# Kernel tuning notes

Measured on AMD Instinct MI355X. Metric: run time of the kernel, lower is better.

## Reference

```python
import jax, jax.numpy as jnp
import numpy as np

NUM_NODES = 100000
NUM_EDGES = 3200000
D_IN, D_HID, D_OUT = 64, 64, 32


def setup_inputs() -> dict:
    key = jax.random.key(0)
    k1, k2, k3, k4, k5 = jax.random.split(key, 5)
    edge_index = jax.random.randint(k1, (2, NUM_EDGES), 0, NUM_NODES, dtype=jnp.int64)
    edge_weight = jax.random.uniform(k2, (NUM_EDGES,), dtype=jnp.float32)
    emb = jax.random.normal(k3, (NUM_NODES, D_IN), dtype=jnp.float32)
    # glorot-ish scaled weights for the two GCNConv layers
    W1 = jax.random.normal(k4, (D_IN, D_HID), dtype=jnp.float32) * (1.0 / np.sqrt(D_IN))
    b1 = jnp.zeros((D_HID,), dtype=jnp.float32)
    W2 = jax.random.normal(k5, (D_HID, D_OUT), dtype=jnp.float32) * (1.0 / np.sqrt(D_HID))
    b2 = jnp.zeros((D_OUT,), dtype=jnp.float32)
    return {"edge_index": edge_index, "edge_weight": edge_weight,
            "emb": emb, "W1": W1, "b1": b1, "W2": W2, "b2": b2}


def reference(edge_index, edge_weight, emb, W1, b1, W2, b2):
    N = emb.shape[0]
    row, col = edge_index[0], edge_index[1]
    # PyG gcn_norm: add self-loops (weight 1.0), symmetric normalization
    loop = jnp.arange(N, dtype=edge_index.dtype)
    row_f = jnp.concatenate([row, loop])
    col_f = jnp.concatenate([col, loop])
    ew_f = jnp.concatenate([edge_weight, jnp.ones((N,), dtype=edge_weight.dtype)])
    deg = jax.ops.segment_sum(ew_f, col_f, num_segments=N)          # [N]
    deg_inv_sqrt = jnp.where(deg > 0, jax.lax.rsqrt(deg), 0.0)      # inf -> 0
    norm = deg_inv_sqrt[row_f] * ew_f * deg_inv_sqrt[col_f]         # [E+N]

    def gcn_conv(x, W, b):
        x = x @ W                                                    # [N, d_out]
        msg = x[row_f] * norm[:, None]                               # [E+N, d_out]
        out = jax.ops.segment_sum(msg, col_f, num_segments=N)       # [N, d_out]
        return out + b

    x = jax.nn.relu(gcn_conv(emb, W1, b1))
    x = gcn_conv(x, W2, b2)
    # F.normalize(p=2, dim=1, eps=1e-12)
    l2 = jnp.linalg.norm(x, axis=1, keepdims=True)
    return x / jnp.maximum(l2, 1e-12)
```

## Files before the change

### kernel.cpp

```cpp
#include <hip/hip_runtime.h>
#include <hip/hip_fp16.h>
#include <math.h>

#define THREADS 256
#define BWIDTH 512
#define BSHIFT 9
#define CHUNK 3125

__global__ void init_kernel(const int* __restrict__ ei32, int* __restrict__ flag,
                            unsigned int* __restrict__ gcnt) {
    int t = threadIdx.x;
    gcnt[t] = 0u;
    if (t == 0) {
        int z = (ei32[1] == 0) + (ei32[3] == 0) + (ei32[5] == 0) + (ei32[7] == 0);
        *flag = (z == 4) ? 1 : 0;
    }
}

__device__ __forceinline__ int edge_at(const void* ei, int is64, size_t idx) {
    return is64 ? (int)((const long long*)ei)[idx] : ((const int*)ei)[idx];
}

__global__ void p1_count_kernel(const void* __restrict__ ei, const int* __restrict__ flag,
                                unsigned int* __restrict__ gcnt, unsigned int* __restrict__ table,
                                int E, int B) {
    __shared__ unsigned int lcnt[256];
    int t = threadIdx.x, b = blockIdx.x;
    lcnt[t] = 0u;
    __syncthreads();
    int is64 = *flag;
    int base = b * CHUNK;
    int end = min(E, base + CHUNK);
    for (int e = base + t; e < end; e += THREADS) {
        int c = edge_at(ei, is64, (size_t)E + e);
        atomicAdd(&lcnt[c >> BSHIFT], 1u);
    }
    __syncthreads();
    if (t < B) table[(size_t)b * 256 + t] = atomicAdd(&gcnt[t], lcnt[t]);
}

__global__ void p2_scan_kernel(const unsigned int* __restrict__ gcnt,
                               unsigned int* __restrict__ bstart, int B, int E) {
    int t = threadIdx.x;
    unsigned int v = (t < B) ? gcnt[t] : 0u;
    unsigned int incl = v;
    int lane = t & 63, wid = t >> 6;
#pragma unroll
    for (int off = 1; off < 64; off <<= 1) {
        unsigned int x = __shfl_up(incl, off);
        if (lane >= off) incl += x;
    }
    __shared__ unsigned int ws4[4];
    if (lane == 63) ws4[wid] = incl;
    __syncthreads();
    unsigned int wb = 0;
    for (int w = 0; w < wid; ++w) wb += ws4[w];
    unsigned int excl = wb + incl - v;
    if (t < B) bstart[t] = excl;
    if (t == 0) bstart[B] = (unsigned int)E;
}

__global__ void p3_scatter_kernel(const void* __restrict__ ei, const float* __restrict__ ew,
                                  const int* __restrict__ flag,
                                  const unsigned int* __restrict__ bstart,
                                  const unsigned int* __restrict__ table,
                                  int2* __restrict__ out, int E, int B) {
    __shared__ int2 stage[CHUNK];
    __shared__ unsigned char lbin[CHUNK];
    __shared__ unsigned short perm[CHUNK];
    __shared__ unsigned int lcnt[256];
    __shared__ unsigned int lstart[256];
    __shared__ unsigned int lcur[256];
    __shared__ int shiftb[256];
    __shared__ unsigned int ws4[4];

    int t = threadIdx.x, b = blockIdx.x;
    lcnt[t] = 0u;
    __syncthreads();
    int is64 = *flag;
    int base = b * CHUNK;
    int end = min(E, base + CHUNK);
    int n = end - base;
    for (int i = t; i < n; i += THREADS) {
        int e = base + i;
        int r = edge_at(ei, is64, (size_t)e);
        int c = edge_at(ei, is64, (size_t)E + e);
        int bin = c >> BSHIFT;
        stage[i] = make_int2(r | ((c & (BWIDTH - 1)) << 17), __float_as_int(ew[e]));
        lbin[i] = (unsigned char)bin;
        atomicAdd(&lcnt[bin], 1u);
    }
    __syncthreads();
    unsigned int v = lcnt[t];
    unsigned int incl = v;
    int lane = t & 63, wid = t >> 6;
#pragma unroll
    for (int off = 1; off < 64; off <<= 1) {
        unsigned int x = __shfl_up(incl, off);
        if (lane >= off) incl += x;
    }
    if (lane == 63) ws4[wid] = incl;
    __syncthreads();
    unsigned int wb = 0;
    for (int w = 0; w < wid; ++w) wb += ws4[w];
    unsigned int excl = wb + incl - v;
    lstart[t] = excl;
    lcur[t] = excl;
    shiftb[t] = (t < B) ? ((int)(bstart[t] + table[(size_t)b * 256 + t]) - (int)excl) : 0;
    __syncthreads();
    for (int i = t; i < n; i += THREADS) {
        unsigned int pos = atomicAdd(&lcur[lbin[i]], 1u);
        perm[pos] = (unsigned short)i;
    }
    __syncthreads();
    for (int k = t; k < n; k += THREADS) {
        int i = perm[k];
        int bin = lbin[i];
        out[(size_t)(shiftb[bin] + k)] = stage[i];
    }
}

__global__ void p5_bucket_kernel(const int2* __restrict__ bucketed,
                                 const unsigned int* __restrict__ bstart,
                                 float* __restrict__ dinv, int* __restrict__ colptr,
                                 int2* __restrict__ csr, int N, int E) {
    __shared__ unsigned int cnt[BWIDTH];
    __shared__ float deg[BWIDTH];
    __shared__ unsigned int cur[BWIDTH];
    __shared__ unsigned int ws4[4];

    int t = threadIdx.x, b = blockIdx.x;
    cnt[t] = 0u; cnt[t + 256] = 0u;
    deg[t] = 0.f; deg[t + 256] = 0.f;
    __syncthreads();
    unsigned int s = bstart[b], e2 = bstart[b + 1];
    for (unsigned int j = s + t; j < e2; j += THREADS) {
        int2 v = bucketed[j];
        unsigned int cl = ((unsigned int)v.x) >> 17;
        atomicAdd(&cnt[cl], 1u);
        atomicAdd(&deg[cl], __int_as_float(v.y));
    }
    __syncthreads();
    unsigned int a0 = cnt[2 * t], a1 = cnt[2 * t + 1];
    unsigned int sum = a0 + a1;
    unsigned int incl = sum;
    int lane = t & 63, wid = t >> 6;
#pragma unroll
    for (int off = 1; off < 64; off <<= 1) {
        unsigned int x = __shfl_up(incl, off);
        if (lane >= off) incl += x;
    }
    if (lane == 63) ws4[wid] = incl;
    __syncthreads();
    unsigned int wb = 0;
    for (int w = 0; w < wid; ++w) wb += ws4[w];
    unsigned int exclT = wb + incl - sum;
    unsigned int e0 = exclT, e1 = exclT + a0;
    int node0 = b << BSHIFT;
    int n0 = node0 + 2 * t, n1 = n0 + 1;
    if (n0 < N) {
        colptr[n0] = (int)(s + e0);
        dinv[n0] = rsqrtf(deg[2 * t] + 1.0f);
    }
    if (n1 < N) {
        colptr[n1] = (int)(s + e1);
        dinv[n1] = rsqrtf(deg[2 * t + 1] + 1.0f);
    }
    cur[2 * t] = s + e0;
    cur[2 * t + 1] = s + e1;
    __syncthreads();
    for (unsigned int j = s + t; j < e2; j += THREADS) {
        int2 v = bucketed[j];
        unsigned int cl = ((unsigned int)v.x) >> 17;
        unsigned int pos = atomicAdd(&cur[cl], 1u);
        csr[pos] = v;
    }
    if (b == 0 && t == 0) colptr[N] = E;
}

__device__ __forceinline__ float ldf(const float* p, size_t i) { return p[i]; }
__device__ __forceinline__ float ldf(const __half* p, size_t i) { return __half2float(p[i]); }

template <typename TIN, int DOUT>
__global__ void gemm_kernel(const TIN* __restrict__ X, const float* __restrict__ W,
                            __half* __restrict__ Y, int N) {
    constexpr int RPB = 256 / DOUT;
    __shared__ float Wl[64 * DOUT];
    __shared__ float Xl[RPB * 64];
    int tid = threadIdx.x;
    for (int i = tid; i < 64 * DOUT; i += 256) Wl[i] = W[i];
    int base = blockIdx.x * RPB;
    for (int i = tid; i < RPB * 64; i += 256) {
        int rr = base + i / 64;
        Xl[i] = (rr < N) ? ldf(X, (size_t)rr * 64 + (i & 63)) : 0.f;
    }
    __syncthreads();
    int r = tid / DOUT, c = tid % DOUT;
    int row = base + r;
    if (row < N) {
        float acc = 0.f;
#pragma unroll
        for (int k = 0; k < 64; ++k) acc = fmaf(Xl[r * 64 + k], Wl[k * DOUT + c], acc);
        Y[(size_t)row * DOUT + c] = __float2half(acc);
    }
}

__global__ void agg1_kernel(const __half* __restrict__ X1, const int* __restrict__ colptr,
                            const int2* __restrict__ csr, const float* __restrict__ dinv,
                            const float* __restrict__ bias, __half* __restrict__ H, int N) {
    int tid = threadIdx.x;
    int node = blockIdx.x * 4 + (tid >> 6);
    int d = tid & 63;
    if (node >= N) return;
    float di = dinv[node];
    float xself = __half2float(X1[(size_t)node * 64 + d]);
    float accE = 0.f;
    int s = colptr[node], e = colptr[node + 1];
    int j = s;
    for (; j + 8 <= e; j += 8) {
        int2 v0 = csr[j + 0], v1 = csr[j + 1], v2 = csr[j + 2], v3 = csr[j + 3];
        int2 v4 = csr[j + 4], v5 = csr[j + 5], v6 = csr[j + 6], v7 = csr[j + 7];
        int r0 = v0.x & 0x1FFFF, r1 = v1.x & 0x1FFFF, r2 = v2.x & 0x1FFFF, r3 = v3.x & 0x1FFFF;
        int r4 = v4.x & 0x1FFFF, r5 = v5.x & 0x1FFFF, r6 = v6.x & 0x1FFFF, r7 = v7.x & 0x1FFFF;
        float w0 = dinv[r0] * __int_as_float(v0.y);
        float w1 = dinv[r1] * __int_as_float(v1.y);
        float w2 = dinv[r2] * __int_as_float(v2.y);
        float w3 = dinv[r3] * __int_as_float(v3.y);
        float w4 = dinv[r4] * __int_as_float(v4.y);
        float w5 = dinv[r5] * __int_as_float(v5.y);
        float w6 = dinv[r6] * __int_as_float(v6.y);
        float w7 = dinv[r7] * __int_as_float(v7.y);
        float x0 = __half2float(X1[(size_t)r0 * 64 + d]);
        float x1 = __half2float(X1[(size_t)r1 * 64 + d]);
        float x2 = __half2float(X1[(size_t)r2 * 64 + d]);
        float x3 = __half2float(X1[(size_t)r3 * 64 + d]);
        float x4 = __half2float(X1[(size_t)r4 * 64 + d]);
        float x5 = __half2float(X1[(size_t)r5 * 64 + d]);
        float x6 = __half2float(X1[(size_t)r6 * 64 + d]);
        float x7 = __half2float(X1[(size_t)r7 * 64 + d]);
        accE = fmaf(w0, x0, accE); accE = fmaf(w1, x1, accE);
        accE = fmaf(w2, x2, accE); accE = fmaf(w3, x3, accE);
        accE = fmaf(w4, x4, accE); accE = fmaf(w5, x5, accE);
        accE = fmaf(w6, x6, accE); accE = fmaf(w7, x7, accE);
    }
    for (; j < e; ++j) {
        int2 v = csr[j];
        int r = v.x & 0x1FFFF;
        accE = fmaf(dinv[r] * __int_as_float(v.y), __half2float(X1[(size_t)r * 64 + d]), accE);
    }
    float acc = bias[d] + di * fmaf(di, xself, accE);
    H[(size_t)node * 64 + d] = __float2half(fmaxf(acc, 0.f));
}

__global__ void agg2_kernel(const __half* __restrict__ X2, const int* __restrict__ colptr,
                            const int2* __restrict__ csr, const float* __restrict__ dinv,
                            const float* __restrict__ bias, float* __restrict__ out, int N) {
    int tid = threadIdx.x;
    int node = blockIdx.x * 8 + (tid >> 5);
    int d = tid & 31;
    if (node >= N) return;
    float di = dinv[node];
    float xself = __half2float(X2[(size_t)node * 32 + d]);
    float accE = 0.f;
    int s = colptr[node], e = colptr[node + 1];
    int j = s;
    for (; j + 8 <= e; j += 8) {
        int2 v0 = csr[j + 0], v1 = csr[j + 1], v2 = csr[j + 2], v3 = csr[j + 3];
        int2 v4 = csr[j + 4], v5 = csr[j + 5], v6 = csr[j + 6], v7 = csr[j + 7];
        int r0 = v0.x & 0x1FFFF, r1 = v1.x & 0x1FFFF, r2 = v2.x & 0x1FFFF, r3 = v3.x & 0x1FFFF;
        int r4 = v4.x & 0x1FFFF, r5 = v5.x & 0x1FFFF, r6 = v6.x & 0x1FFFF, r7 = v7.x & 0x1FFFF;
        float w0 = dinv[r0] * __int_as_float(v0.y);
        float w1 = dinv[r1] * __int_as_float(v1.y);
        float w2 = dinv[r2] * __int_as_float(v2.y);
        float w3 = dinv[r3] * __int_as_float(v3.y);
        float w4 = dinv[r4] * __int_as_float(v4.y);
        float w5 = dinv[r5] * __int_as_float(v5.y);
        float w6 = dinv[r6] * __int_as_float(v6.y);
        float w7 = dinv[r7] * __int_as_float(v7.y);
        float x0 = __half2float(X2[(size_t)r0 * 32 + d]);
        float x1 = __half2float(X2[(size_t)r1 * 32 + d]);
        float x2 = __half2float(X2[(size_t)r2 * 32 + d]);
        float x3 = __half2float(X2[(size_t)r3 * 32 + d]);
        float x4 = __half2float(X2[(size_t)r4 * 32 + d]);
        float x5 = __half2float(X2[(size_t)r5 * 32 + d]);
        float x6 = __half2float(X2[(size_t)r6 * 32 + d]);
        float x7 = __half2float(X2[(size_t)r7 * 32 + d]);
        accE = fmaf(w0, x0, accE); accE = fmaf(w1, x1, accE);
        accE = fmaf(w2, x2, accE); accE = fmaf(w3, x3, accE);
        accE = fmaf(w4, x4, accE); accE = fmaf(w5, x5, accE);
        accE = fmaf(w6, x6, accE); accE = fmaf(w7, x7, accE);
    }
    for (; j < e; ++j) {
        int2 v = csr[j];
        int r = v.x & 0x1FFFF;
        accE = fmaf(dinv[r] * __int_as_float(v.y), __half2float(X2[(size_t)r * 32 + d]), accE);
    }
    float acc = bias[d] + di * fmaf(di, xself, accE);
    float ss = acc * acc;
#pragma unroll
    for (int m = 16; m >= 1; m >>= 1) ss += __shfl_xor(ss, m);
    float l2 = sqrtf(ss);
    out[(size_t)node * 32 + d] = acc / fmaxf(l2, 1e-12f);
}

extern "C" void kernel_launch(void* const* d_in, const int* in_sizes, int n_in,
                              void* d_out, int out_size, void* d_ws, size_t ws_size,
                              hipStream_t stream) {
    const void* ei = d_in[0];
    const float* ew = (const float*)d_in[1];
    const float* emb = (const float*)d_in[2];
    const float* W1 = (const float*)d_in[3];
    const float* b1 = (const float*)d_in[4];
    const float* W2 = (const float*)d_in[5];
    const float* b2 = (const float*)d_in[6];
    float* outp = (float*)d_out;

    int E = in_sizes[0] / 2;
    int N = in_sizes[2] / 64;
    int B = (N + BWIDTH - 1) >> BSHIFT;
    int GP = (E + CHUNK - 1) / CHUNK;

    char* p = (char*)d_ws;
    auto alloc = [&](size_t bytes) {
        void* q = (void*)p;
        p += (bytes + 255) & ~(size_t)255;
        return q;
    };
    unsigned int* gcnt   = (unsigned int*)alloc(256 * 4);
    unsigned int* bstart = (unsigned int*)alloc(257 * 4);
    int*          flag   = (int*)alloc(256);
    unsigned int* table  = (unsigned int*)alloc((size_t)GP * 256 * 4);
    int2*   bucketed = (int2*)alloc((size_t)E * 8);
    int2*   csr      = (int2*)alloc((size_t)E * 8);
    float*  dinv     = (float*)alloc((size_t)N * 4);
    int*    colptr   = (int*)alloc(((size_t)N + 1) * 4);
    __half* X1h      = (__half*)alloc((size_t)N * 64 * 2);
    __half* H        = (__half*)alloc((size_t)N * 64 * 2);
    __half* X2h      = X1h;

    init_kernel<<<1, 256, 0, stream>>>((const int*)ei, flag, gcnt);
    p1_count_kernel<<<GP, THREADS, 0, stream>>>(ei, flag, gcnt, table, E, B);
    p2_scan_kernel<<<1, 256, 0, stream>>>(gcnt, bstart, B, E);
    p3_scatter_kernel<<<GP, THREADS, 0, stream>>>(ei, ew, flag, bstart, table,
                                                  bucketed, E, B);
    p5_bucket_kernel<<<B, THREADS, 0, stream>>>(bucketed, bstart, dinv, colptr, csr, N, E);
    gemm_kernel<float, 64><<<(N + 3) / 4, THREADS, 0, stream>>>(emb, W1, X1h, N);
    agg1_kernel<<<(N + 3) / 4, THREADS, 0, stream>>>(X1h, colptr, csr, dinv, b1, H, N);
    gemm_kernel<__half, 32><<<(N + 7) / 8, THREADS, 0, stream>>>(H, W2, X2h, N);
    agg2_kernel<<<(N + 7) / 8, THREADS, 0, stream>>>(X2h, colptr, csr, dinv, b2, outp, N);
}
```

Measured before the change: 351.6 us.

## Fold degree normalization into GEMM and CSR weights; vectorize aggregation lanes

Precomputes the column-side normalization into CSR edge weights during bucketing and scales GEMM outputs by the row-side inverse sqrt degree. This removes the per-edge random gather of dinv in both aggregation kernels. The aggregation kernels are restructured so each lane loads half2 feature pairs and lane groups process different edges, then reduce with shuffles. The cost is extra multiplies in bucketing and GEMM, plus cross-lane reductions.

```diff
diff --git a/kernel.cpp b/kernel.cpp
--- a/kernel.cpp
+++ b/kernel.cpp
@@ -69,7 +69,6 @@
     __shared__ unsigned char lbin[CHUNK];
     __shared__ unsigned short perm[CHUNK];
     __shared__ unsigned int lcnt[256];
-    __shared__ unsigned int lstart[256];
     __shared__ unsigned int lcur[256];
     __shared__ int shiftb[256];
     __shared__ unsigned int ws4[4];
@@ -104,7 +103,6 @@
     unsigned int wb = 0;
     for (int w = 0; w < wid; ++w) wb += ws4[w];
     unsigned int excl = wb + incl - v;
-    lstart[t] = excl;
     lcur[t] = excl;
     shiftb[t] = (t < B) ? ((int)(bstart[t] + table[(size_t)b * 256 + t]) - (int)excl) : 0;
     __syncthreads();
@@ -158,14 +156,12 @@
     unsigned int e0 = exclT, e1 = exclT + a0;
     int node0 = b << BSHIFT;
     int n0 = node0 + 2 * t, n1 = n0 + 1;
-    if (n0 < N) {
-        colptr[n0] = (int)(s + e0);
-        dinv[n0] = rsqrtf(deg[2 * t] + 1.0f);
-    }
-    if (n1 < N) {
-        colptr[n1] = (int)(s + e1);
-        dinv[n1] = rsqrtf(deg[2 * t + 1] + 1.0f);
-    }
+    float d0 = rsqrtf(deg[2 * t] + 1.0f);
+    float d1 = rsqrtf(deg[2 * t + 1] + 1.0f);
+    if (n0 < N) { colptr[n0] = (int)(s + e0); dinv[n0] = d0; }
+    if (n1 < N) { colptr[n1] = (int)(s + e1); dinv[n1] = d1; }
+    deg[2 * t] = d0;
+    deg[2 * t + 1] = d1;
     cur[2 * t] = s + e0;
     cur[2 * t + 1] = s + e1;
     __syncthreads();
@@ -173,7 +169,8 @@
         int2 v = bucketed[j];
         unsigned int cl = ((unsigned int)v.x) >> 17;
         unsigned int pos = atomicAdd(&cur[cl], 1u);
-        csr[pos] = v;
+        float w = __int_as_float(v.y) * deg[cl];
+        csr[pos] = make_int2(v.x, __float_as_int(w));
     }
     if (b == 0 && t == 0) colptr[N] = E;
 }
@@ -183,7 +180,7 @@
 
 template <typename TIN, int DOUT>
 __global__ void gemm_kernel(const TIN* __restrict__ X, const float* __restrict__ W,
-                            __half* __restrict__ Y, int N) {
+                            const float* __restrict__ dinv, __half* __restrict__ Y, int N) {
     constexpr int RPB = 256 / DOUT;
     __shared__ float Wl[64 * DOUT];
     __shared__ float Xl[RPB * 64];
@@ -201,7 +198,7 @@
         float acc = 0.f;
 #pragma unroll
         for (int k = 0; k < 64; ++k) acc = fmaf(Xl[r * 64 + k], Wl[k * DOUT + c], acc);
-        Y[(size_t)row * DOUT + c] = __float2half(acc);
+        Y[(size_t)row * DOUT + c] = __float2half(acc * dinv[row]);
     }
 }
 
@@ -210,97 +207,111 @@
                             const float* __restrict__ bias, __half* __restrict__ H, int N) {
     int tid = threadIdx.x;
     int node = blockIdx.x * 4 + (tid >> 6);
-    int d = tid & 63;
     if (node >= N) return;
-    float di = dinv[node];
-    float xself = __half2float(X1[(size_t)node * 64 + d]);
-    float accE = 0.f;
+    int lane = tid & 63;
+    int eo = lane >> 5;
+    int dp = lane & 31;
     int s = colptr[node], e = colptr[node + 1];
+    float acc0 = 0.f, acc1 = 0.f;
     int j = s;
-    for (; j + 8 <= e; j += 8) {
-        int2 v0 = csr[j + 0], v1 = csr[j + 1], v2 = csr[j + 2], v3 = csr[j + 3];
-        int2 v4 = csr[j + 4], v5 = csr[j + 5], v6 = csr[j + 6], v7 = csr[j + 7];
-        int r0 = v0.x & 0x1FFFF, r1 = v1.x & 0x1FFFF, r2 = v2.x & 0x1FFFF, r3 = v3.x & 0x1FFFF;
-        int r4 = v4.x & 0x1FFFF, r5 = v5.x & 0x1FFFF, r6 = v6.x & 0x1FFFF, r7 = v7.x & 0x1FFFF;
-        float w0 = dinv[r0] * __int_as_float(v0.y);
-        float w1 = dinv[r1] * __int_as_float(v1.y);
-        float w2 = dinv[r2] * __int_as_float(v2.y);
-        float w3 = dinv[r3] * __int_as_float(v3.y);
-        float w4 = dinv[r4] * __int_as_float(v4.y);
-        float w5 = dinv[r5] * __int_as_float(v5.y);
-        float w6 = dinv[r6] * __int_as_float(v6.y);
-        float w7 = dinv[r7] * __int_as_float(v7.y);
-        float x0 = __half2float(X1[(size_t)r0 * 64 + d]);
-        float x1 = __half2float(X1[(size_t)r1 * 64 + d]);
-        float x2 = __half2float(X1[(size_t)r2 * 64 + d]);
-        float x3 = __half2float(X1[(size_t)r3 * 64 + d]);
-        float x4 = __half2float(X1[(size_t)r4 * 64 + d]);
-        float x5 = __half2float(X1[(size_t)r5 * 64 + d]);
-        float x6 = __half2float(X1[(size_t)r6 * 64 + d]);
-        float x7 = __half2float(X1[(size_t)r7 * 64 + d]);
-        accE = fmaf(w0, x0, accE); accE = fmaf(w1, x1, accE);
-        accE = fmaf(w2, x2, accE); accE = fmaf(w3, x3, accE);
-        accE = fmaf(w4, x4, accE); accE = fmaf(w5, x5, accE);
-        accE = fmaf(w6, x6, accE); accE = fmaf(w7, x7, accE);
-    }
-    for (; j < e; ++j) {
-        int2 v = csr[j];
-        int r = v.x & 0x1FFFF;
-        accE = fmaf(dinv[r] * __int_as_float(v.y), __half2float(X1[(size_t)r * 64 + d]), accE);
-    }
-    float acc = bias[d] + di * fmaf(di, xself, accE);
-    H[(size_t)node * 64 + d] = __float2half(fmaxf(acc, 0.f));
+    while (j + 16 <= e) {
+        int2 vv[8];
+#pragma unroll
+        for (int k = 0; k < 8; ++k) vv[k] = csr[j + 2 * k + eo];
+        __half2 hh[8];
+#pragma unroll
+        for (int k = 0; k < 8; ++k) {
+            int r = vv[k].x & 0x1FFFF;
+            hh[k] = *(const __half2*)(X1 + ((size_t)r << 6) + (dp << 1));
+        }
+#pragma unroll
+        for (int k = 0; k < 8; ++k) {
+            float2 x = __half22float2(hh[k]);
+            float w = __int_as_float(vv[k].y);
+            acc0 = fmaf(w, x.x, acc0);
+            acc1 = fmaf(w, x.y, acc1);
+        }
+        j += 16;
+    }
+    for (; j < e; j += 2) {
+        int jj = j + eo;
+        float w = 0.f;
+        int r = 0;
+        if (jj < e) { int2 v = csr[jj]; r = v.x & 0x1FFFF; w = __int_as_float(v.y); }
+        __half2 h = *(const __half2*)(X1 + ((size_t)r << 6) + (dp << 1));
+        float2 x = __half22float2(h);
+        acc0 = fmaf(w, x.x, acc0);
+        acc1 = fmaf(w, x.y, acc1);
+    }
+    acc0 += __shfl_xor(acc0, 32);
+    acc1 += __shfl_xor(acc1, 32);
+    if (eo == 0) {
+        float di = dinv[node];
+        __half2 hs = *(const __half2*)(X1 + ((size_t)node << 6) + (dp << 1));
+        float2 xs = __half22float2(hs);
+        float a0 = fmaxf(bias[2 * dp + 0] + fmaf(di, xs.x, acc0), 0.f);
+        float a1 = fmaxf(bias[2 * dp + 1] + fmaf(di, xs.y, acc1), 0.f);
+        *(__half2*)(H + ((size_t)node << 6) + (dp << 1)) = __floats2half2_rn(a0, a1);
+    }
 }
 
 __global__ void agg2_kernel(const __half* __restrict__ X2, const int* __restrict__ colptr,
                             const int2* __restrict__ csr, const float* __restrict__ dinv,
                             const float* __restrict__ bias, float* __restrict__ out, int N) {
     int tid = threadIdx.x;
-    int node = blockIdx.x * 8 + (tid >> 5);
-    int d = tid & 31;
+    int node = blockIdx.x * 4 + (tid >> 6);
     if (node >= N) return;
+    int lane = tid & 63;
+    int eo = lane >> 4;
+    int dp = lane & 15;
+    int s = colptr[node], e = colptr[node + 1];
+    float acc0 = 0.f, acc1 = 0.f;
+    int j = s;
+    while (j + 16 <= e) {
+        int2 vv[4];
+#pragma unroll
+        for (int k = 0; k < 4; ++k) vv[k] = csr[j + 4 * k + eo];
+        __half2 hh[4];
+#pragma unroll
+        for (int k = 0; k < 4; ++k) {
+            int r = vv[k].x & 0x1FFFF;
+            hh[k] = *(const __half2*)(X2 + ((size_t)r << 5) + (dp << 1));
+        }
+#pragma unroll
+        for (int k = 0; k < 4; ++k) {
+            float2 x = __half22float2(hh[k]);
+            float w = __int_as_float(vv[k].y);
+            acc0 = fmaf(w, x.x, acc0);
+            acc1 = fmaf(w, x.y, acc1);
+        }
+        j += 16;
+    }
+    for (; j < e; j += 4) {
+        int jj = j + eo;
+        float w = 0.f;
+        int r = 0;
+        if (jj < e) { int2 v = csr[jj]; r = v.x & 0x1FFFF; w = __int_as_float(v.y); }
+        __half2 h = *(const __half2*)(X2 + ((size_t)r << 5) + (dp << 1));
+        float2 x = __half22float2(h);
+        acc0 = fmaf(w, x.x, acc0);
+        acc1 = fmaf(w, x.y, acc1);
+    }
+    acc0 += __shfl_xor(acc0, 16);
+    acc1 += __shfl_xor(acc1, 16);
+    acc0 += __shfl_xor(acc0, 32);
+    acc1 += __shfl_xor(acc1, 32);
     float di = dinv[node];
-    float xself = __half2float(X2[(size_t)node * 32 + d]);
-    float accE = 0.f;
-    int s = colptr[node], e = colptr[node + 1];
-    int j = s;
-    for (; j + 8 <= e; j += 8) {
-        int2 v0 = csr[j + 0], v1 = csr[j + 1], v2 = csr[j + 2], v3 = csr[j + 3];
-        int2 v4 = csr[j + 4], v5 = csr[j + 5], v6 = csr[j + 6], v7 = csr[j + 7];
-        int r0 = v0.x & 0x1FFFF, r1 = v1.x & 0x1FFFF, r2 = v2.x & 0x1FFFF, r3 = v3.x & 0x1FFFF;
-        int r4 = v4.x & 0x1FFFF, r5 = v5.x & 0x1FFFF, r6 = v6.x & 0x1FFFF, r7 = v7.x & 0x1FFFF;
-        float w0 = dinv[r0] * __int_as_float(v0.y);
-        float w1 = dinv[r1] * __int_as_float(v1.y);
-        float w2 = dinv[r2] * __int_as_float(v2.y);
-        float w3 = dinv[r3] * __int_as_float(v3.y);
-        float w4 = dinv[r4] * __int_as_float(v4.y);
-        float w5 = dinv[r5] * __int_as_float(v5.y);
-        float w6 = dinv[r6] * __int_as_float(v6.y);
-        float w7 = dinv[r7] * __int_as_float(v7.y);
-        float x0 = __half2float(X2[(size_t)r0 * 32 + d]);
-        float x1 = __half2float(X2[(size_t)r1 * 32 + d]);
-        float x2 = __half2float(X2[(size_t)r2 * 32 + d]);
-        float x3 = __half2float(X2[(size_t)r3 * 32 + d]);
-        float x4 = __half2float(X2[(size_t)r4 * 32 + d]);
-        float x5 = __half2float(X2[(size_t)r5 * 32 + d]);
-        float x6 = __half2float(X2[(size_t)r6 * 32 + d]);
-        float x7 = __half2float(X2[(size_t)r7 * 32 + d]);
-        accE = fmaf(w0, x0, accE); accE = fmaf(w1, x1, accE);
-        accE = fmaf(w2, x2, accE); accE = fmaf(w3, x3, accE);
-        accE = fmaf(w4, x4, accE); accE = fmaf(w5, x5, accE);
-        accE = fmaf(w6, x6, accE); accE = fmaf(w7, x7, accE);
-    }
-    for (; j < e; ++j) {
-        int2 v = csr[j];
-        int r = v.x & 0x1FFFF;
-        accE = fmaf(dinv[r] * __int_as_float(v.y), __half2float(X2[(size_t)r * 32 + d]), accE);
-    }
-    float acc = bias[d] + di * fmaf(di, xself, accE);
-    float ss = acc * acc;
-#pragma unroll
-    for (int m = 16; m >= 1; m >>= 1) ss += __shfl_xor(ss, m);
-    float l2 = sqrtf(ss);
-    out[(size_t)node * 32 + d] = acc / fmaxf(l2, 1e-12f);
+    __half2 hs = *(const __half2*)(X2 + ((size_t)node << 5) + (dp << 1));
+    float2 xs = __half22float2(hs);
+    float a0 = bias[2 * dp + 0] + fmaf(di, xs.x, acc0);
+    float a1 = bias[2 * dp + 1] + fmaf(di, xs.y, acc1);
+    float ss = fmaf(a0, a0, a1 * a1);
+#pragma unroll
+    for (int m = 1; m <= 8; m <<= 1) ss += __shfl_xor(ss, m);
+    float inv = 1.f / fmaxf(sqrtf(ss), 1e-12f);
+    if (eo == 0) {
+        *(float2*)(out + ((size_t)node << 5) + (dp << 1)) = make_float2(a0 * inv, a1 * inv);
+    }
 }
 
 extern "C" void kernel_launch(void* const* d_in, const int* in_sizes, int n_in,
@@ -331,7 +342,7 @@
     int*          flag   = (int*)alloc(256);
     unsigned int* table  = (unsigned int*)alloc((size_t)GP * 256 * 4);
     int2*   bucketed = (int2*)alloc((size_t)E * 8);
-    int2*   csr      = (int2*)alloc((size_t)E * 8);
+    int2*   csr      = (int2*)alloc(((size_t)E + 16) * 8);
     float*  dinv     = (float*)alloc((size_t)N * 4);
     int*    colptr   = (int*)alloc(((size_t)N + 1) * 4);
     __half* X1h      = (__half*)alloc((size_t)N * 64 * 2);
@@ -344,8 +355,8 @@
     p3_scatter_kernel<<<GP, THREADS, 0, stream>>>(ei, ew, flag, bstart, table,
                                                   bucketed, E, B);
     p5_bucket_kernel<<<B, THREADS, 0, stream>>>(bucketed, bstart, dinv, colptr, csr, N, E);
-    gemm_kernel<float, 64><<<(N + 3) / 4, THREADS, 0, stream>>>(emb, W1, X1h, N);
+    gemm_kernel<float, 64><<<(N + 3) / 4, THREADS, 0, stream>>>(emb, W1, dinv, X1h, N);
     agg1_kernel<<<(N + 3) / 4, THREADS, 0, stream>>>(X1h, colptr, csr, dinv, b1, H, N);
-    gemm_kernel<__half, 32><<<(N + 7) / 8, THREADS, 0, stream>>>(H, W2, X2h, N);
-    agg2_kernel<<<(N + 7) / 8, THREADS, 0, stream>>>(X2h, colptr, csr, dinv, b2, outp, N);
-}
+    gemm_kernel<__half, 32><<<(N + 7) / 8, THREADS, 0, stream>>>(H, W2, dinv, X2h, N);
+    agg2_kernel<<<(N + 3) / 4, THREADS, 0, stream>>>(X2h, colptr, csr, dinv, b2, outp, N);
+}
```

New measurement: 327.1 us. 1.07x faster.
